# Performance work log

Measured on AMD Instinct MI355X. Metric: run time of the kernel, lower is better.

The kernel has to match this reference:

```python
import jax, jax.numpy as jnp
import numpy as np

NUM_EXPERTS = 8
NUM_ROWS = 8192
HIDDEN = 2048
INTER = 2048
TOPK = 2


def setup_inputs() -> dict:
    key = jax.random.key(0)
    ks = jax.random.split(key, 5)
    x = jax.random.normal(ks[0], (NUM_ROWS, HIDDEN), dtype=jnp.float32)
    router_probs = jax.random.uniform(ks[1], (NUM_ROWS, NUM_EXPERTS), dtype=jnp.float32)
    # parameters ~ U(-0.1, 0.1) as in nn.init.uniform_
    fc1 = jax.random.uniform(ks[2], (NUM_EXPERTS, HIDDEN, INTER), minval=-0.1, maxval=0.1, dtype=jnp.float32)
    fc2 = jax.random.uniform(ks[3], (NUM_EXPERTS, INTER, HIDDEN), minval=-0.1, maxval=0.1, dtype=jnp.float32)
    fc3 = jax.random.uniform(ks[4], (NUM_EXPERTS, HIDDEN, INTER), minval=-0.1, maxval=0.1, dtype=jnp.float32)
    return {"x": x, "router_probs": router_probs, "fc1": fc1, "fc2": fc2, "fc3": fc3}


def reference(x, router_probs, fc1, fc2, fc3):
    # top-k routing + renormalize chosen probs
    topk_probs, topk_idx = jax.lax.top_k(router_probs, TOPK)  # [N, K]
    topk_probs = topk_probs / jnp.sum(topk_probs, axis=1, keepdims=True)
    # combine weight per (token, expert): scatter-add normalized probs
    n = x.shape[0]
    cw = jnp.zeros((n, NUM_EXPERTS), dtype=x.dtype)
    cw = cw.at[jnp.arange(n)[:, None], topk_idx].add(topk_probs)  # [N, E]
    # loop over fixed, small expert set (structurally distinct weights)
    out = jnp.zeros_like(x)
    for e in range(NUM_EXPERTS):
        h1 = x @ fc1[e]                      # [N, inter]
        h3 = x @ fc3[e]                      # [N, inter]
        act = jax.nn.silu(h1) * h3           # SwiGLU
        out = out + cw[:, e:e + 1] * (act @ fc2[e])
    return out
```

## Files before the change

kernel.cpp:

```cpp
#include <hip/hip_runtime.h>
#include <hip/hip_bf16.h>
#include <stdint.h>

#define NEXP 8
#define NROWS 8192
#define HID 2048
#define INTERN 2048
#define CAP 8192
#define KDIM 2048

typedef __attribute__((ext_vector_type(4))) float f32x4;
typedef __attribute__((ext_vector_type(8))) short bf16x8;

__device__ __forceinline__ unsigned short f2bf(float f) {
  union { float f; uint32_t u; } v; v.f = f;
  uint32_t u = v.u;
  uint32_t r = (u + 0x7fffu + ((u >> 16) & 1u)) >> 16;
  return (unsigned short)r;
}
__device__ __forceinline__ float bf2f(unsigned short u) {
  union { uint32_t u; float f; } v; v.u = (uint32_t)u << 16; return v.f;
}
__device__ __forceinline__ void gload16(const unsigned short* g, char* l) {
  __builtin_amdgcn_global_load_lds((const __attribute__((address_space(1))) void*)g,
                                   (__attribute__((address_space(3))) void*)l,
                                   16, 0, 0);
}

__global__ __launch_bounds__(256) void xcast_kernel(const float* __restrict__ x,
                                                    unsigned short* __restrict__ xb) {
  size_t i = ((size_t)blockIdx.x * 256 + threadIdx.x) * 8;
  size_t stride = (size_t)gridDim.x * 256 * 8;
  const size_t tot = (size_t)NROWS * HID;
  for (; i < tot; i += stride) {
    float4 a = *reinterpret_cast<const float4*>(x + i);
    float4 b = *reinterpret_cast<const float4*>(x + i + 4);
    unsigned short u[8];
    u[0] = f2bf(a.x); u[1] = f2bf(a.y); u[2] = f2bf(a.z); u[3] = f2bf(a.w);
    u[4] = f2bf(b.x); u[5] = f2bf(b.y); u[6] = f2bf(b.z); u[7] = f2bf(b.w);
    *reinterpret_cast<int4*>(xb + i) = *reinterpret_cast<const int4*>(u);
  }
}

__global__ void router_kernel(const float* __restrict__ probs,
                              int* __restrict__ cnt,
                              int* __restrict__ brow,
                              float* __restrict__ bw) {
  int row = blockIdx.x * blockDim.x + threadIdx.x;
  if (row >= NROWS) return;
  float p[8];
#pragma unroll
  for (int j = 0; j < 8; j++) p[j] = probs[row * 8 + j];
  int i1 = 0; float v1 = p[0];
#pragma unroll
  for (int j = 1; j < 8; j++) if (p[j] > v1) { v1 = p[j]; i1 = j; }
  int i2 = -1; float v2 = -1e30f;
#pragma unroll
  for (int j = 0; j < 8; j++) if (j != i1 && p[j] > v2) { v2 = p[j]; i2 = j; }
  float s = v1 + v2;
  float w1 = v1 / s, w2 = v2 / s;
  int pos1 = atomicAdd(&cnt[i1], 1);
  brow[i1 * CAP + pos1] = row; bw[i1 * CAP + pos1] = w1;
  int pos2 = atomicAdd(&cnt[i2], 1);
  brow[i2 * CAP + pos2] = row; bw[i2 * CAP + pos2] = w2;
}

__global__ void offsets_kernel(const int* __restrict__ cnt, int* __restrict__ ofs) {
  if (threadIdx.x == 0 && blockIdx.x == 0) {
    int a = 0;
    for (int e = 0; e < NEXP; e++) { ofs[e] = a; a += cnt[e]; }
  }
}

__global__ __launch_bounds__(256) void transpose_cast_kernel(const float* __restrict__ src,
                                                             unsigned short* __restrict__ dst) {
  __shared__ float tile[64][65];
  const int e = blockIdx.z;
  const int k0 = blockIdx.y * 64;
  const int n0 = blockIdx.x * 64;
  const float* s = src + (size_t)e * KDIM * KDIM;
  unsigned short* d = dst + (size_t)e * KDIM * KDIM;
  const int t = threadIdx.x;
  const int rr = t >> 4, cc = (t & 15) * 4;
#pragma unroll
  for (int i = 0; i < 4; i++) {
    float4 v = *reinterpret_cast<const float4*>(s + (size_t)(k0 + rr + i * 16) * KDIM + n0 + cc);
    tile[rr + i * 16][cc + 0] = v.x; tile[rr + i * 16][cc + 1] = v.y;
    tile[rr + i * 16][cc + 2] = v.z; tile[rr + i * 16][cc + 3] = v.w;
  }
  __syncthreads();
  const int n = t >> 2, kk0 = (t & 3) * 16;
  unsigned short u[16];
#pragma unroll
  for (int j = 0; j < 16; j++) u[j] = f2bf(tile[kk0 + j][n]);
  *reinterpret_cast<int4*>(d + (size_t)(n0 + n) * KDIM + k0 + kk0 + 0) = *reinterpret_cast<const int4*>(&u[0]);
  *reinterpret_cast<int4*>(d + (size_t)(n0 + n) * KDIM + k0 + kk0 + 8) = *reinterpret_cast<const int4*>(&u[8]);
}

__global__ __launch_bounds__(256, 2)
void gemm13_kernel(const unsigned short* __restrict__ A,
                   const unsigned short* __restrict__ W1,
                   const unsigned short* __restrict__ W3,
                   const int* __restrict__ cnt, const int* __restrict__ ofs,
                   const int* __restrict__ brow,
                   unsigned short* __restrict__ act) {
  const int e = blockIdx.z, mt = blockIdx.y, nt = blockIdx.x;
  const int Me = cnt[e];
  if (mt * 128 >= Me) return;
  __shared__ unsigned short As[128 * 64];
  __shared__ unsigned short B1s[128 * 64];
  __shared__ unsigned short B3s[128 * 64];
  __shared__ int ridx[128];
  const int t = threadIdx.x, lane = t & 63, wave = t >> 6;
  const int oe = ofs[e];
  if (t < 128) {
    int sl = mt * 128 + t;
    ridx[t] = (sl < Me) ? brow[e * CAP + sl] : 0;
  }
  __syncthreads();

  const int srow = t >> 3;
  const int kg = ((t & 7) ^ (srow & 7)) * 8;
  const unsigned short* pA0 = A + (size_t)ridx[srow +  0] * KDIM + kg;
  const unsigned short* pA1 = A + (size_t)ridx[srow + 32] * KDIM + kg;
  const unsigned short* pA2 = A + (size_t)ridx[srow + 64] * KDIM + kg;
  const unsigned short* pA3 = A + (size_t)ridx[srow + 96] * KDIM + kg;
  const unsigned short* pB0 = W1 + (size_t)e * KDIM * KDIM + (size_t)(nt * 128 + srow) * KDIM + kg;
  const ptrdiff_t dW = W3 - W1;
  char* dA  = (char*)As  + wave * 1024;
  char* dB1 = (char*)B1s + wave * 1024;
  char* dB3 = (char*)B3s + wave * 1024;

  const int wm = wave >> 1, wn = wave & 1;
  const int l15 = lane & 15, kq = lane >> 4;
  const int c0 = (kq * 16) ^ ((l15 & 7) << 4);
  const int aoff = (wm * 64 + l15) * 128;
  const int boff = (wn * 64 + l15) * 128;

  f32x4 acc1[4][4] = {};
  f32x4 acc3[4][4] = {};

  for (int k0 = 0; k0 < KDIM; k0 += 64) {
    gload16(pA0, dA);                    gload16(pA1, dA + 4096);
    gload16(pA2, dA + 8192);             gload16(pA3, dA + 12288);
    gload16(pB0,                dB1);    gload16(pB0 +  32 * KDIM, dB1 + 4096);
    gload16(pB0 + 64 * KDIM,    dB1 + 8192); gload16(pB0 + 96 * KDIM, dB1 + 12288);
    gload16(pB0 + dW,           dB3);    gload16(pB0 + dW + 32 * KDIM, dB3 + 4096);
    gload16(pB0 + dW + 64 * KDIM, dB3 + 8192); gload16(pB0 + dW + 96 * KDIM, dB3 + 12288);
    pA0 += 64; pA1 += 64; pA2 += 64; pA3 += 64; pB0 += 64;
    __syncthreads();

#pragma unroll
    for (int h = 0; h < 2; h++) {
      const int ch = h ? (c0 ^ 64) : c0;
      bf16x8 af[4], bf[4];
#pragma unroll
      for (int i = 0; i < 4; i++)
        af[i] = *reinterpret_cast<const bf16x8*>((const char*)As + aoff + i * 2048 + ch);
#pragma unroll
      for (int i = 0; i < 4; i++)
        bf[i] = *reinterpret_cast<const bf16x8*>((const char*)B1s + boff + i * 2048 + ch);
#pragma unroll
      for (int mi = 0; mi < 4; mi++)
#pragma unroll
        for (int ni = 0; ni < 4; ni++)
          acc1[mi][ni] = __builtin_amdgcn_mfma_f32_16x16x32_bf16(af[mi], bf[ni], acc1[mi][ni], 0, 0, 0);
#pragma unroll
      for (int i = 0; i < 4; i++)
        bf[i] = *reinterpret_cast<const bf16x8*>((const char*)B3s + boff + i * 2048 + ch);
#pragma unroll
      for (int mi = 0; mi < 4; mi++)
#pragma unroll
        for (int ni = 0; ni < 4; ni++)
          acc3[mi][ni] = __builtin_amdgcn_mfma_f32_16x16x32_bf16(af[mi], bf[ni], acc3[mi][ni], 0, 0, 0);
    }
    __syncthreads();
  }

  const int slot0 = oe + mt * 128;
#pragma unroll
  for (int mi = 0; mi < 4; mi++) {
#pragma unroll
    for (int ni = 0; ni < 4; ni++) {
      const int coln = nt * 128 + wn * 64 + ni * 16 + l15;
#pragma unroll
      for (int r = 0; r < 4; r++) {
        const int lrow = wm * 64 + mi * 16 + kq * 4 + r;
        if (mt * 128 + lrow < Me) {
          float h1 = acc1[mi][ni][r];
          float h3 = acc3[mi][ni][r];
          float sig = 1.f / (1.f + __expf(-h1));
          act[(size_t)(slot0 + lrow) * KDIM + coln] = f2bf(h1 * sig * h3);
        }
      }
    }
  }
}

__global__ __launch_bounds__(256, 2)
void gemm2_kernel(const unsigned short* __restrict__ A,
                  const unsigned short* __restrict__ W,
                  const int* __restrict__ cnt, const int* __restrict__ ofs,
                  const int* __restrict__ brow, const float* __restrict__ bw,
                  float* __restrict__ out) {
  const int e = blockIdx.z, mt = blockIdx.y, nt = blockIdx.x;
  const int Me = cnt[e];
  if (mt * 128 >= Me) return;
  __shared__ unsigned short As[128 * 64];
  __shared__ unsigned short Bs[128 * 64];
  __shared__ int ridx[128];
  __shared__ float rww[128];
  const int t = threadIdx.x, lane = t & 63, wave = t >> 6;
  const int oe = ofs[e];
  if (t < 128) {
    int sl = mt * 128 + t;
    int ok = sl < Me;
    ridx[t] = ok ? brow[e * CAP + sl] : 0;
    rww[t] = ok ? bw[e * CAP + sl] : 0.f;
  }
  __syncthreads();

  const int srow = t >> 3;
  const int kg = ((t & 7) ^ (srow & 7)) * 8;
  int s;
  const unsigned short *pA0, *pA1, *pA2, *pA3;
  s = mt * 128 + srow +  0; if (s >= Me) s = 0; pA0 = A + (size_t)(oe + s) * KDIM + kg;
  s = mt * 128 + srow + 32; if (s >= Me) s = 0; pA1 = A + (size_t)(oe + s) * KDIM + kg;
  s = mt * 128 + srow + 64; if (s >= Me) s = 0; pA2 = A + (size_t)(oe + s) * KDIM + kg;
  s = mt * 128 + srow + 96; if (s >= Me) s = 0; pA3 = A + (size_t)(oe + s) * KDIM + kg;
  const unsigned short* pB0 = W + (size_t)e * KDIM * KDIM + (size_t)(nt * 128 + srow) * KDIM + kg;
  char* dA = (char*)As + wave * 1024;
  char* dB = (char*)Bs + wave * 1024;

  const int wm = wave >> 1, wn = wave & 1;
  const int l15 = lane & 15, kq = lane >> 4;
  const int c0 = (kq * 16) ^ ((l15 & 7) << 4);
  const int aoff = (wm * 64 + l15) * 128;
  const int boff = (wn * 64 + l15) * 128;

  f32x4 acc[4][4] = {};

  for (int k0 = 0; k0 < KDIM; k0 += 64) {
    gload16(pA0, dA);         gload16(pA1, dA + 4096);
    gload16(pA2, dA + 8192);  gload16(pA3, dA + 12288);
    gload16(pB0,             dB);        gload16(pB0 + 32 * KDIM, dB + 4096);
    gload16(pB0 + 64 * KDIM, dB + 8192); gload16(pB0 + 96 * KDIM, dB + 12288);
    pA0 += 64; pA1 += 64; pA2 += 64; pA3 += 64; pB0 += 64;
    __syncthreads();

#pragma unroll
    for (int h = 0; h < 2; h++) {
      const int ch = h ? (c0 ^ 64) : c0;
      bf16x8 af[4], bf[4];
#pragma unroll
      for (int i = 0; i < 4; i++) {
        af[i] = *reinterpret_cast<const bf16x8*>((const char*)As + aoff + i * 2048 + ch);
        bf[i] = *reinterpret_cast<const bf16x8*>((const char*)Bs + boff + i * 2048 + ch);
      }
#pragma unroll
      for (int mi = 0; mi < 4; mi++)
#pragma unroll
        for (int ni = 0; ni < 4; ni++)
          acc[mi][ni] = __builtin_amdgcn_mfma_f32_16x16x32_bf16(af[mi], bf[ni], acc[mi][ni], 0, 0, 0);
    }
    __syncthreads();
  }

#pragma unroll
  for (int mi = 0; mi < 4; mi++) {
#pragma unroll
    for (int ni = 0; ni < 4; ni++) {
      const int coln = nt * 128 + wn * 64 + ni * 16 + l15;
#pragma unroll
      for (int r = 0; r < 4; r++) {
        const int lrow = wm * 64 + mi * 16 + kq * 4 + r;
        if (mt * 128 + lrow < Me) {
          float v = acc[mi][ni][r] * rww[lrow];
          unsafeAtomicAdd(&out[(size_t)ridx[lrow] * HID + coln], v);
        }
      }
    }
  }
}

extern "C" void kernel_launch(void* const* d_in, const int* in_sizes, int n_in,
                              void* d_out, int out_size, void* d_ws, size_t ws_size,
                              hipStream_t stream) {
  const float* x     = (const float*)d_in[0];
  const float* probs = (const float*)d_in[1];
  const float* fc1   = (const float*)d_in[2];
  const float* fc2   = (const float*)d_in[3];
  const float* fc3   = (const float*)d_in[4];
  float* out = (float*)d_out;

  char* ws = (char*)d_ws;
  const size_t WSZ = (size_t)NEXP * HID * INTERN * 2;
  unsigned short* wt1 = (unsigned short*)(ws);
  unsigned short* wt3 = (unsigned short*)(ws + WSZ);
  unsigned short* wt2 = (unsigned short*)(ws + 2 * WSZ);
  unsigned short* act = (unsigned short*)(ws + 3 * WSZ);
  unsigned short* xb  = (unsigned short*)(ws + 4 * WSZ);
  char* rbase = ws + 4 * WSZ + (size_t)NROWS * HID * 2;
  int*   brow = (int*)  (rbase);
  float* bw   = (float*)(rbase + (size_t)NEXP * CAP * 4);
  int*   cnt  = (int*)  (rbase + 2 * (size_t)NEXP * CAP * 4);
  int*   ofs  = (int*)  (rbase + 2 * (size_t)NEXP * CAP * 4 + 64);

  hipMemsetAsync(d_out, 0, (size_t)out_size * sizeof(float), stream);
  hipMemsetAsync(cnt, 0, 64, stream);

  xcast_kernel<<<2048, 256, 0, stream>>>(x, xb);
  transpose_cast_kernel<<<dim3(32, 32, 8), 256, 0, stream>>>(fc1, wt1);
  transpose_cast_kernel<<<dim3(32, 32, 8), 256, 0, stream>>>(fc3, wt3);
  transpose_cast_kernel<<<dim3(32, 32, 8), 256, 0, stream>>>(fc2, wt2);
  router_kernel<<<NROWS / 256, 256, 0, stream>>>(probs, cnt, brow, bw);
  offsets_kernel<<<1, 64, 0, stream>>>(cnt, ofs);

  gemm13_kernel<<<dim3(INTERN / 128, CAP / 128, NEXP), 256, 0, stream>>>(xb, wt1, wt3, cnt, ofs, brow, act);
  gemm2_kernel<<<dim3(HID / 128, CAP / 128, NEXP), 256, 0, stream>>>(act, wt2, cnt, ofs, brow, bw, out);
}
```

Before: 731.3 us.

## Triple-buffer LDS with BK=32 and async prefetch in both MoE GEMMs

Both grouped GEMM kernels move from a single-buffered BK=64 loop, which waits at a barrier after every load, to a three-stage ring of LDS buffers with BK=32 tiles. Tile k+2 is prefetched through global_load_lds while tile k is computed, and explicit vmcnt waits plus s_barrier replace __syncthreads. The XOR swizzle and LDS offsets are redone for the 64-byte row stride. This hides global-memory latency behind MFMA work, but LDS use rises (72KB for gemm13) and each tile does less compute per barrier.

```diff
diff --git a/kernel.cpp b/kernel.cpp
--- a/kernel.cpp
+++ b/kernel.cpp
@@ -97,6 +97,8 @@
   *reinterpret_cast<int4*>(d + (size_t)(n0 + n) * KDIM + k0 + kk0 + 8) = *reinterpret_cast<const int4*>(&u[8]);
 }
 
+#define B13 24576
+
 __global__ __launch_bounds__(256, 2)
 void gemm13_kernel(const unsigned short* __restrict__ A,
                    const unsigned short* __restrict__ W1,
@@ -107,9 +109,7 @@
   const int e = blockIdx.z, mt = blockIdx.y, nt = blockIdx.x;
   const int Me = cnt[e];
   if (mt * 128 >= Me) return;
-  __shared__ unsigned short As[128 * 64];
-  __shared__ unsigned short B1s[128 * 64];
-  __shared__ unsigned short B3s[128 * 64];
+  __shared__ __align__(128) char lds[3 * B13];
   __shared__ int ridx[128];
   const int t = threadIdx.x, lane = t & 63, wave = t >> 6;
   const int oe = ofs[e];
@@ -119,63 +119,68 @@
   }
   __syncthreads();
 
-  const int srow = t >> 3;
-  const int kg = ((t & 7) ^ (srow & 7)) * 8;
-  const unsigned short* pA0 = A + (size_t)ridx[srow +  0] * KDIM + kg;
-  const unsigned short* pA1 = A + (size_t)ridx[srow + 32] * KDIM + kg;
-  const unsigned short* pA2 = A + (size_t)ridx[srow + 64] * KDIM + kg;
-  const unsigned short* pA3 = A + (size_t)ridx[srow + 96] * KDIM + kg;
-  const unsigned short* pB0 = W1 + (size_t)e * KDIM * KDIM + (size_t)(nt * 128 + srow) * KDIM + kg;
+  const int srow = t >> 2;
+  const int kg = ((t & 3) ^ ((srow >> 1) & 3)) * 8;
+  const unsigned short* pA0 = A + (size_t)ridx[srow] * KDIM + kg;
+  const unsigned short* pA1 = A + (size_t)ridx[srow + 64] * KDIM + kg;
+  const unsigned short* pB  = W1 + (size_t)e * KDIM * KDIM + (size_t)(nt * 128 + srow) * KDIM + kg;
   const ptrdiff_t dW = W3 - W1;
-  char* dA  = (char*)As  + wave * 1024;
-  char* dB1 = (char*)B1s + wave * 1024;
-  char* dB3 = (char*)B3s + wave * 1024;
+  const int wdst = wave * 1024;
 
   const int wm = wave >> 1, wn = wave & 1;
   const int l15 = lane & 15, kq = lane >> 4;
-  const int c0 = (kq * 16) ^ ((l15 & 7) << 4);
-  const int aoff = (wm * 64 + l15) * 128;
-  const int boff = (wn * 64 + l15) * 128;
+  const int c0 = (kq ^ ((l15 >> 1) & 3)) << 4;
+  const int aoff  = (wm * 64 + l15) * 64 + c0;
+  const int b1off = 8192 + (wn * 64 + l15) * 64 + c0;
+  const int b3off = 16384 + (wn * 64 + l15) * 64 + c0;
 
   f32x4 acc1[4][4] = {};
   f32x4 acc3[4][4] = {};
 
-  for (int k0 = 0; k0 < KDIM; k0 += 64) {
-    gload16(pA0, dA);                    gload16(pA1, dA + 4096);
-    gload16(pA2, dA + 8192);             gload16(pA3, dA + 12288);
-    gload16(pB0,                dB1);    gload16(pB0 +  32 * KDIM, dB1 + 4096);
-    gload16(pB0 + 64 * KDIM,    dB1 + 8192); gload16(pB0 + 96 * KDIM, dB1 + 12288);
-    gload16(pB0 + dW,           dB3);    gload16(pB0 + dW + 32 * KDIM, dB3 + 4096);
-    gload16(pB0 + dW + 64 * KDIM, dB3 + 8192); gload16(pB0 + dW + 96 * KDIM, dB3 + 12288);
-    pA0 += 64; pA1 += 64; pA2 += 64; pA3 += 64; pB0 += 64;
-    __syncthreads();
-
-#pragma unroll
-    for (int h = 0; h < 2; h++) {
-      const int ch = h ? (c0 ^ 64) : c0;
-      bf16x8 af[4], bf[4];
-#pragma unroll
-      for (int i = 0; i < 4; i++)
-        af[i] = *reinterpret_cast<const bf16x8*>((const char*)As + aoff + i * 2048 + ch);
-#pragma unroll
-      for (int i = 0; i < 4; i++)
-        bf[i] = *reinterpret_cast<const bf16x8*>((const char*)B1s + boff + i * 2048 + ch);
-#pragma unroll
-      for (int mi = 0; mi < 4; mi++)
-#pragma unroll
-        for (int ni = 0; ni < 4; ni++)
-          acc1[mi][ni] = __builtin_amdgcn_mfma_f32_16x16x32_bf16(af[mi], bf[ni], acc1[mi][ni], 0, 0, 0);
-#pragma unroll
-      for (int i = 0; i < 4; i++)
-        bf[i] = *reinterpret_cast<const bf16x8*>((const char*)B3s + boff + i * 2048 + ch);
-#pragma unroll
-      for (int mi = 0; mi < 4; mi++)
-#pragma unroll
-        for (int ni = 0; ni < 4; ni++)
-          acc3[mi][ni] = __builtin_amdgcn_mfma_f32_16x16x32_bf16(af[mi], bf[ni], acc3[mi][ni], 0, 0, 0);
-    }
-    __syncthreads();
-  }
+#define STAGE13(bo) do { \
+    char* d_ = lds + (bo) + wdst; \
+    gload16(pA0, d_);              gload16(pA1, d_ + 4096); \
+    gload16(pB, d_ + 8192);        gload16(pB + 64 * KDIM, d_ + 12288); \
+    gload16(pB + dW, d_ + 16384);  gload16(pB + dW + 64 * KDIM, d_ + 20480); \
+    pA0 += 32; pA1 += 32; pB += 32; } while (0)
+
+#define COMP13(bo) do { \
+    const char* ab_ = lds + (bo); \
+    bf16x8 af[4], bf[4]; \
+    _Pragma("unroll") for (int i = 0; i < 4; i++) \
+      af[i] = *reinterpret_cast<const bf16x8*>(ab_ + aoff + i * 1024); \
+    _Pragma("unroll") for (int i = 0; i < 4; i++) \
+      bf[i] = *reinterpret_cast<const bf16x8*>(ab_ + b1off + i * 1024); \
+    _Pragma("unroll") for (int mi = 0; mi < 4; mi++) \
+      _Pragma("unroll") for (int ni = 0; ni < 4; ni++) \
+        acc1[mi][ni] = __builtin_amdgcn_mfma_f32_16x16x32_bf16(af[mi], bf[ni], acc1[mi][ni], 0, 0, 0); \
+    _Pragma("unroll") for (int i = 0; i < 4; i++) \
+      bf[i] = *reinterpret_cast<const bf16x8*>(ab_ + b3off + i * 1024); \
+    _Pragma("unroll") for (int mi = 0; mi < 4; mi++) \
+      _Pragma("unroll") for (int ni = 0; ni < 4; ni++) \
+        acc3[mi][ni] = __builtin_amdgcn_mfma_f32_16x16x32_bf16(af[mi], bf[ni], acc3[mi][ni], 0, 0, 0); \
+  } while (0)
+
+  STAGE13(0); STAGE13(B13);
+  asm volatile("s_waitcnt vmcnt(6)" ::: "memory");
+  asm volatile("s_barrier" ::: "memory");
+
+  int ro = 0, so = 2 * B13;
+  for (int kt = 0; kt < 62; ++kt) {
+    STAGE13(so);
+    COMP13(ro);
+    asm volatile("s_waitcnt vmcnt(6) lgkmcnt(0)" ::: "memory");
+    asm volatile("s_barrier" ::: "memory");
+    ro = (ro == 2 * B13) ? 0 : ro + B13;
+    so = (so == 2 * B13) ? 0 : so + B13;
+  }
+  COMP13(ro);
+  asm volatile("s_waitcnt vmcnt(0) lgkmcnt(0)" ::: "memory");
+  asm volatile("s_barrier" ::: "memory");
+  ro = (ro == 2 * B13) ? 0 : ro + B13;
+  COMP13(ro);
+#undef STAGE13
+#undef COMP13
 
   const int slot0 = oe + mt * 128;
 #pragma unroll
@@ -197,6 +202,8 @@
   }
 }
 
+#define B2 16384
+
 __global__ __launch_bounds__(256, 2)
 void gemm2_kernel(const unsigned short* __restrict__ A,
                   const unsigned short* __restrict__ W,
@@ -206,8 +213,7 @@
   const int e = blockIdx.z, mt = blockIdx.y, nt = blockIdx.x;
   const int Me = cnt[e];
   if (mt * 128 >= Me) return;
-  __shared__ unsigned short As[128 * 64];
-  __shared__ unsigned short Bs[128 * 64];
+  __shared__ __align__(128) char lds[3 * B2];
   __shared__ int ridx[128];
   __shared__ float rww[128];
   const int t = threadIdx.x, lane = t & 63, wave = t >> 6;
@@ -220,51 +226,60 @@
   }
   __syncthreads();
 
-  const int srow = t >> 3;
-  const int kg = ((t & 7) ^ (srow & 7)) * 8;
+  const int srow = t >> 2;
+  const int kg = ((t & 3) ^ ((srow >> 1) & 3)) * 8;
   int s;
-  const unsigned short *pA0, *pA1, *pA2, *pA3;
-  s = mt * 128 + srow +  0; if (s >= Me) s = 0; pA0 = A + (size_t)(oe + s) * KDIM + kg;
-  s = mt * 128 + srow + 32; if (s >= Me) s = 0; pA1 = A + (size_t)(oe + s) * KDIM + kg;
-  s = mt * 128 + srow + 64; if (s >= Me) s = 0; pA2 = A + (size_t)(oe + s) * KDIM + kg;
-  s = mt * 128 + srow + 96; if (s >= Me) s = 0; pA3 = A + (size_t)(oe + s) * KDIM + kg;
-  const unsigned short* pB0 = W + (size_t)e * KDIM * KDIM + (size_t)(nt * 128 + srow) * KDIM + kg;
-  char* dA = (char*)As + wave * 1024;
-  char* dB = (char*)Bs + wave * 1024;
+  const unsigned short *pA0, *pA1;
+  s = mt * 128 + srow;      if (s >= Me) s = 0; pA0 = A + (size_t)(oe + s) * KDIM + kg;
+  s = mt * 128 + srow + 64; if (s >= Me) s = 0; pA1 = A + (size_t)(oe + s) * KDIM + kg;
+  const unsigned short* pB = W + (size_t)e * KDIM * KDIM + (size_t)(nt * 128 + srow) * KDIM + kg;
+  const int wdst = wave * 1024;
 
   const int wm = wave >> 1, wn = wave & 1;
   const int l15 = lane & 15, kq = lane >> 4;
-  const int c0 = (kq * 16) ^ ((l15 & 7) << 4);
-  const int aoff = (wm * 64 + l15) * 128;
-  const int boff = (wn * 64 + l15) * 128;
+  const int c0 = (kq ^ ((l15 >> 1) & 3)) << 4;
+  const int aoff = (wm * 64 + l15) * 64 + c0;
+  const int boff = 8192 + (wn * 64 + l15) * 64 + c0;
 
   f32x4 acc[4][4] = {};
 
-  for (int k0 = 0; k0 < KDIM; k0 += 64) {
-    gload16(pA0, dA);         gload16(pA1, dA + 4096);
-    gload16(pA2, dA + 8192);  gload16(pA3, dA + 12288);
-    gload16(pB0,             dB);        gload16(pB0 + 32 * KDIM, dB + 4096);
-    gload16(pB0 + 64 * KDIM, dB + 8192); gload16(pB0 + 96 * KDIM, dB + 12288);
-    pA0 += 64; pA1 += 64; pA2 += 64; pA3 += 64; pB0 += 64;
-    __syncthreads();
-
-#pragma unroll
-    for (int h = 0; h < 2; h++) {
-      const int ch = h ? (c0 ^ 64) : c0;
-      bf16x8 af[4], bf[4];
-#pragma unroll
-      for (int i = 0; i < 4; i++) {
-        af[i] = *reinterpret_cast<const bf16x8*>((const char*)As + aoff + i * 2048 + ch);
-        bf[i] = *reinterpret_cast<const bf16x8*>((const char*)Bs + boff + i * 2048 + ch);
-      }
-#pragma unroll
-      for (int mi = 0; mi < 4; mi++)
-#pragma unroll
-        for (int ni = 0; ni < 4; ni++)
-          acc[mi][ni] = __builtin_amdgcn_mfma_f32_16x16x32_bf16(af[mi], bf[ni], acc[mi][ni], 0, 0, 0);
-    }
-    __syncthreads();
-  }
+#define STAGE2(bo) do { \
+    char* d_ = lds + (bo) + wdst; \
+    gload16(pA0, d_);       gload16(pA1, d_ + 4096); \
+    gload16(pB, d_ + 8192); gload16(pB + 64 * KDIM, d_ + 12288); \
+    pA0 += 32; pA1 += 32; pB += 32; } while (0)
+
+#define COMP2(bo) do { \
+    const char* ab_ = lds + (bo); \
+    bf16x8 af[4], bf[4]; \
+    _Pragma("unroll") for (int i = 0; i < 4; i++) { \
+      af[i] = *reinterpret_cast<const bf16x8*>(ab_ + aoff + i * 1024); \
+      bf[i] = *reinterpret_cast<const bf16x8*>(ab_ + boff + i * 1024); } \
+    _Pragma("unroll") for (int mi = 0; mi < 4; mi++) \
+      _Pragma("unroll") for (int ni = 0; ni < 4; ni++) \
+        acc[mi][ni] = __builtin_amdgcn_mfma_f32_16x16x32_bf16(af[mi], bf[ni], acc[mi][ni], 0, 0, 0); \
+  } while (0)
+
+  STAGE2(0); STAGE2(B2);
+  asm volatile("s_waitcnt vmcnt(4)" ::: "memory");
+  asm volatile("s_barrier" ::: "memory");
+
+  int ro = 0, so = 2 * B2;
+  for (int kt = 0; kt < 62; ++kt) {
+    STAGE2(so);
+    COMP2(ro);
+    asm volatile("s_waitcnt vmcnt(4) lgkmcnt(0)" ::: "memory");
+    asm volatile("s_barrier" ::: "memory");
+    ro = (ro == 2 * B2) ? 0 : ro + B2;
+    so = (so == 2 * B2) ? 0 : so + B2;
+  }
+  COMP2(ro);
+  asm volatile("s_waitcnt vmcnt(0) lgkmcnt(0)" ::: "memory");
+  asm volatile("s_barrier" ::: "memory");
+  ro = (ro == 2 * B2) ? 0 : ro + B2;
+  COMP2(ro);
+#undef STAGE2
+#undef COMP2
 
 #pragma unroll
   for (int mi = 0; mi < 4; mi++) {
```

New measurement: 828.3 us. 1.13x slower.

## Double-buffer gemm2 LDS with BK=32 stages to overlap loads and MFMA

Applied to the files above, without the earlier changes.

Rewrites the gemm2 main loop to use two LDS buffers with a K-step of 32. The global-to-LDS load of the next tile is issued before computing on the current tile, so memory and MFMA work overlap, with one barrier per step instead of two. The LDS swizzle is changed to fit the 64-byte row layout, and launch bounds are raised to 3 blocks per CU to add occupancy. The risk is that the smaller K-step doubles the number of barrier steps, and three blocks per CU may force register spills.

```diff
diff --git a/kernel.cpp b/kernel.cpp
--- a/kernel.cpp
+++ b/kernel.cpp
@@ -197,7 +197,9 @@
   }
 }
 
-__global__ __launch_bounds__(256, 2)
+#define GB2 16384
+
+__global__ __launch_bounds__(256, 3)
 void gemm2_kernel(const unsigned short* __restrict__ A,
                   const unsigned short* __restrict__ W,
                   const int* __restrict__ cnt, const int* __restrict__ ofs,
@@ -206,8 +208,7 @@
   const int e = blockIdx.z, mt = blockIdx.y, nt = blockIdx.x;
   const int Me = cnt[e];
   if (mt * 128 >= Me) return;
-  __shared__ unsigned short As[128 * 64];
-  __shared__ unsigned short Bs[128 * 64];
+  __shared__ __align__(128) char lds[2 * GB2];
   __shared__ int ridx[128];
   __shared__ float rww[128];
   const int t = threadIdx.x, lane = t & 63, wave = t >> 6;
@@ -220,51 +221,53 @@
   }
   __syncthreads();
 
-  const int srow = t >> 3;
-  const int kg = ((t & 7) ^ (srow & 7)) * 8;
+  const int srow = t >> 2;
+  const int kg = ((t & 3) ^ ((srow >> 1) & 3)) * 8;
   int s;
-  const unsigned short *pA0, *pA1, *pA2, *pA3;
-  s = mt * 128 + srow +  0; if (s >= Me) s = 0; pA0 = A + (size_t)(oe + s) * KDIM + kg;
-  s = mt * 128 + srow + 32; if (s >= Me) s = 0; pA1 = A + (size_t)(oe + s) * KDIM + kg;
-  s = mt * 128 + srow + 64; if (s >= Me) s = 0; pA2 = A + (size_t)(oe + s) * KDIM + kg;
-  s = mt * 128 + srow + 96; if (s >= Me) s = 0; pA3 = A + (size_t)(oe + s) * KDIM + kg;
-  const unsigned short* pB0 = W + (size_t)e * KDIM * KDIM + (size_t)(nt * 128 + srow) * KDIM + kg;
-  char* dA = (char*)As + wave * 1024;
-  char* dB = (char*)Bs + wave * 1024;
+  const unsigned short *pA0, *pA1;
+  s = mt * 128 + srow;      if (s >= Me) s = 0; pA0 = A + (size_t)(oe + s) * KDIM + kg;
+  s = mt * 128 + srow + 64; if (s >= Me) s = 0; pA1 = A + (size_t)(oe + s) * KDIM + kg;
+  const unsigned short* pB = W + (size_t)e * KDIM * KDIM + (size_t)(nt * 128 + srow) * KDIM + kg;
+  const int wdst = wave * 1024;
 
   const int wm = wave >> 1, wn = wave & 1;
   const int l15 = lane & 15, kq = lane >> 4;
-  const int c0 = (kq * 16) ^ ((l15 & 7) << 4);
-  const int aoff = (wm * 64 + l15) * 128;
-  const int boff = (wn * 64 + l15) * 128;
+  const int c0 = (kq ^ ((l15 >> 1) & 3)) << 4;
+  const int aoff = (wm * 64 + l15) * 64 + c0;
+  const int boff = 8192 + (wn * 64 + l15) * 64 + c0;
 
   f32x4 acc[4][4] = {};
 
-  for (int k0 = 0; k0 < KDIM; k0 += 64) {
-    gload16(pA0, dA);         gload16(pA1, dA + 4096);
-    gload16(pA2, dA + 8192);  gload16(pA3, dA + 12288);
-    gload16(pB0,             dB);        gload16(pB0 + 32 * KDIM, dB + 4096);
-    gload16(pB0 + 64 * KDIM, dB + 8192); gload16(pB0 + 96 * KDIM, dB + 12288);
-    pA0 += 64; pA1 += 64; pA2 += 64; pA3 += 64; pB0 += 64;
-    __syncthreads();
-
-#pragma unroll
-    for (int h = 0; h < 2; h++) {
-      const int ch = h ? (c0 ^ 64) : c0;
-      bf16x8 af[4], bf[4];
-#pragma unroll
-      for (int i = 0; i < 4; i++) {
-        af[i] = *reinterpret_cast<const bf16x8*>((const char*)As + aoff + i * 2048 + ch);
-        bf[i] = *reinterpret_cast<const bf16x8*>((const char*)Bs + boff + i * 2048 + ch);
-      }
-#pragma unroll
-      for (int mi = 0; mi < 4; mi++)
-#pragma unroll
-        for (int ni = 0; ni < 4; ni++)
-          acc[mi][ni] = __builtin_amdgcn_mfma_f32_16x16x32_bf16(af[mi], bf[ni], acc[mi][ni], 0, 0, 0);
-    }
-    __syncthreads();
-  }
+#define STAGE2(bo) do { \
+    char* d_ = lds + (bo) + wdst; \
+    gload16(pA0, d_);       gload16(pA1, d_ + 4096); \
+    gload16(pB, d_ + 8192); gload16(pB + 64 * KDIM, d_ + 12288); \
+    pA0 += 32; pA1 += 32; pB += 32; } while (0)
+
+#define COMP2(bo) do { \
+    bf16x8 af[4], bf[4]; \
+    _Pragma("unroll") for (int i = 0; i < 4; i++) { \
+      af[i] = *reinterpret_cast<const bf16x8*>(lds + (bo) + aoff + i * 1024); \
+      bf[i] = *reinterpret_cast<const bf16x8*>(lds + (bo) + boff + i * 1024); } \
+    _Pragma("unroll") for (int mi = 0; mi < 4; mi++) \
+      _Pragma("unroll") for (int ni = 0; ni < 4; ni++) \
+        acc[mi][ni] = __builtin_amdgcn_mfma_f32_16x16x32_bf16(af[mi], bf[ni], acc[mi][ni], 0, 0, 0); \
+  } while (0)
+#define SYNC2 do { \
+    asm volatile("s_waitcnt vmcnt(0) lgkmcnt(0)" ::: "memory"); \
+    asm volatile("s_barrier" ::: "memory"); } while (0)
+
+  STAGE2(0);
+  SYNC2;
+  for (int kt = 0; kt < 31; ++kt) {
+    STAGE2(GB2);  COMP2(0);    SYNC2;
+    STAGE2(0);    COMP2(GB2);  SYNC2;
+  }
+  STAGE2(GB2);  COMP2(0);  SYNC2;
+  COMP2(GB2);
+#undef STAGE2
+#undef COMP2
+#undef SYNC2
 
 #pragma unroll
   for (int mi = 0; mi < 4; mi++) {
```

Measured after the change: 771.8 us. 1.06x slower.
